# Optimization experiments

Measured on AMD Instinct MI355X. Metric: run time of the kernel, lower is better.

Reference implementation:

```python
import jax, jax.numpy as jnp
import numpy as np

FSIZE = 128   # fsize
ANUM = 16     # number of agents
CNUM = 2048   # number of cities
BATCH = 64


def setup_inputs() -> dict:
    key = jax.random.key(0)
    ks = jax.random.split(key, 6)
    f = FSIZE
    N = CNUM + 2 * ANUM
    s = 0.02
    return {
        "nfeature": jax.random.normal(ks[0], (BATCH, f, N), jnp.float32),
        # torch Linear weights are [out, in]
        "Wg": jax.random.normal(ks[1], (f, 4 * f), jnp.float32) * s,   # glb_embedding
        "bg": jnp.zeros((f,), jnp.float32),
        "Wc": jax.random.normal(ks[2], (3 * f, 2 * f), jnp.float32) * s,  # city_embedding
        "bc": jnp.zeros((3 * f,), jnp.float32),
        "Wa": jax.random.normal(ks[3], (f, 3 * f), jnp.float32) * s,   # agent_embedding
        "ba": jnp.zeros((f,), jnp.float32),
        "Wp": jax.random.normal(ks[4], (f, f), jnp.float32) * s,       # project_out
        "bp": jnp.zeros((f,), jnp.float32),
        "step": 1,
        "anum": ANUM,
    }


def reference(nfeature, Wg, bg, Wc, bc, Wa, ba, Wp, bp, step, anum):
    nf = jnp.transpose(nfeature, (0, 2, 1))  # [B, N, f]
    B, N, f = nf.shape
    cnum = N - 2 * anum
    city = nf[:, :cnum]                       # [B, cnum, f]
    a_start = nf[:, cnum:cnum + anum]         # [B, anum, f]
    a_end = nf[:, cnum + anum:]               # [B, anum, f]

    # global context via max pooling over segments -> glb_embedding
    glb = jnp.concatenate([nf.max(1), city.max(1), a_start.max(1), a_end.max(1)], axis=1)  # [B, 4f]
    deglb = (glb @ Wg.T + bg)[:, None, :]     # [B, 1, f]

    # mean-pooled global context -> same glb_embedding -> free agent token
    ave = jnp.concatenate([nf.mean(1), city.mean(1), a_start.mean(1), a_end.mean(1)], axis=1)
    free_agent = (ave @ Wg.T + bg)[:, None, :]  # [B, 1, f]

    # city keys/values/logit-keys: x, y, z
    city_feat = jnp.concatenate([jnp.broadcast_to(deglb, (B, cnum, f)), city], axis=2)  # [B, cnum, 2f]
    xyz = city_feat @ Wc.T + bc               # [B, cnum, 3f]
    x, y, z = jnp.split(xyz, 3, axis=2)       # each [B, cnum, f]

    # agent queries
    agent_feat = jnp.concatenate(
        [jnp.broadcast_to(deglb, (B, anum, f)), a_start, a_end], axis=2)  # [B, anum, 3f]
    af = agent_feat @ Wa.T + ba               # [B, anum, f]
    if step > 0:
        af = jnp.concatenate([af, free_agent], axis=1)  # [B, anum+1, f]

    scale = 1.0 / jnp.sqrt(jnp.float32(f))
    ucj = jnp.einsum('baf,bcf->bac', af, x) * scale           # [B, A, cnum]
    new_af = jnp.einsum('bac,bcf->baf', jax.nn.softmax(ucj, axis=2), y)
    new_af = new_af @ Wp.T + bp                                # project_out
    logits = jnp.tanh(jnp.einsum('baf,bcf->bac', new_af, z) * scale) * 10.0  # [B, A, cnum]
    probs = jax.nn.softmax(jnp.transpose(logits, (0, 2, 1)), axis=2)         # [B, cnum, A]
    return probs
```

## Files before the change

### kernel.cpp

```cpp
#include <hip/hip_runtime.h>
#include <math.h>

#define F 128
#define NTOT 2080
#define CN 2048
#define AN 16
#define NA 17

__device__ __forceinline__ float wmax(float v){
  #pragma unroll
  for(int m=32;m;m>>=1) v = fmaxf(v, __shfl_xor(v, m, 64));
  return v;
}
__device__ __forceinline__ float wsum(float v){
  #pragma unroll
  for(int m=32;m;m>>=1) v += __shfl_xor(v, m, 64);
  return v;
}

__global__ __launch_bounds__(256) void k0t_transpose(
      const float* __restrict__ Wg, const float* __restrict__ Wc,
      const float* __restrict__ Wp, const float* __restrict__ Wa,
      float* __restrict__ WgT, float* __restrict__ WcT,
      float* __restrict__ WpT, float* __restrict__ WaT){
  __shared__ float tile[32][33];
  const int z = blockIdx.z;
  const float* src; float* dst; int R, C;
  if(z==0){ src=Wg; dst=WgT; R=128; C=512; }
  else if(z==1){ src=Wc; dst=WcT; R=384; C=256; }
  else if(z==2){ src=Wp; dst=WpT; R=128; C=128; }
  else { src=Wa; dst=WaT; R=128; C=384; }
  const int c0 = blockIdx.x*32, r0 = blockIdx.y*32;
  if(c0>=C || r0>=R) return;
  const int tx = threadIdx.x&31, ty = threadIdx.x>>5;
  #pragma unroll
  for(int rr=0;rr<4;rr++)
    tile[ty+rr*8][tx] = src[(size_t)(r0+ty+rr*8)*C + c0 + tx];
  __syncthreads();
  #pragma unroll
  for(int rr=0;rr<4;rr++)
    dst[(size_t)(c0+ty+rr*8)*R + r0 + tx] = tile[tx][ty+rr*8];
}

__global__ __launch_bounds__(128) void k0a_wpy(const float* __restrict__ Wp, const float* __restrict__ Wc,
                                               float* __restrict__ Wpy){
  const int k = blockIdx.x, i = threadIdx.x;
  float acc = 0.f;
  const float* wp = Wp + (size_t)k*F;
  for(int j=0;j<F;j++) acc += wp[j]*Wc[(size_t)(128+j)*256 + 128 + i];
  Wpy[k*F+i] = acc;
}

__global__ __launch_bounds__(128) void k0b_m1(const float* __restrict__ Wc, const float* __restrict__ Wpy,
                                              float* __restrict__ M1){
  const int jc = blockIdx.x, i = threadIdx.x;
  float acc = 0.f;
  for(int k=0;k<F;k++) acc += Wc[(size_t)(256+k)*256 + 128 + jc]*Wpy[k*F+i];
  M1[jc*F+i] = acc;
}

__global__ __launch_bounds__(256) void k1_reduce(const float* __restrict__ nf,
                                                 float* __restrict__ glb, float* __restrict__ ave){
  const int j = blockIdx.x, b = blockIdx.y, tid = threadIdx.x;
  const float4* row = (const float4*)(nf + (size_t)(b*F + j)*NTOT);
  float cmax=-INFINITY, csum=0.f, smax=-INFINITY, ssum=0.f, emax=-INFINITY, esum=0.f;
  for(int n4 = tid; n4 < 520; n4 += 256){
    float4 v = row[n4];
    float mx = fmaxf(fmaxf(v.x,v.y), fmaxf(v.z,v.w));
    float sm = (v.x+v.y)+(v.z+v.w);
    if(n4 < 512){ cmax=fmaxf(cmax,mx); csum+=sm; }
    else if(n4 < 516){ smax=fmaxf(smax,mx); ssum+=sm; }
    else { emax=fmaxf(emax,mx); esum+=sm; }
  }
  __shared__ float red[4][6];
  cmax=wmax(cmax); csum=wsum(csum); smax=wmax(smax); ssum=wsum(ssum); emax=wmax(emax); esum=wsum(esum);
  const int lane = tid&63, wid = tid>>6;
  if(lane==0){ red[wid][0]=cmax; red[wid][1]=csum; red[wid][2]=smax; red[wid][3]=ssum; red[wid][4]=emax; red[wid][5]=esum; }
  __syncthreads();
  if(tid==0){
    float cM=red[0][0], cS=red[0][1], sM=red[0][2], sS=red[0][3], eM=red[0][4], eS=red[0][5];
    for(int w=1;w<4;w++){ cM=fmaxf(cM,red[w][0]); cS+=red[w][1]; sM=fmaxf(sM,red[w][2]); sS+=red[w][3]; eM=fmaxf(eM,red[w][4]); eS+=red[w][5]; }
    const int gb = b*4*F;
    glb[gb + j]       = fmaxf(cM, fmaxf(sM,eM));
    glb[gb + F + j]   = cM;
    glb[gb + 2*F + j] = sM;
    glb[gb + 3*F + j] = eM;
    float tS = cS+sS+eS;
    ave[gb + j]       = tS / 2080.f;
    ave[gb + F + j]   = cS / 2048.f;
    ave[gb + 2*F + j] = sS / 16.f;
    ave[gb + 3*F + j] = eS / 16.f;
  }
}

__global__ __launch_bounds__(256) void k2a_prep(
    const float* __restrict__ WgT, const float* __restrict__ bg,
    const float* __restrict__ WcT, const float* __restrict__ Wc, const float* __restrict__ bc,
    const float* __restrict__ WpT, const float* __restrict__ bp,
    const float* __restrict__ Wpy,
    const float* __restrict__ glb, const float* __restrict__ ave,
    float* __restrict__ deglb_g, float* __restrict__ fa_g, float* __restrict__ cx,
    float* __restrict__ czc, float* __restrict__ vz, float* __restrict__ szc){
  const int b = blockIdx.x, tid = threadIdx.x;
  __shared__ float glb_s[512], ave_s[512];
  __shared__ float deglb_s[F], cvec_s[3*F], cpy_s[F];
  for(int i=tid;i<512;i+=256){ glb_s[i]=glb[b*512+i]; ave_s[i]=ave[b*512+i]; }
  __syncthreads();
  {
    const int j = tid&127;
    const float* src = (tid<128)? glb_s : ave_s;
    float a0=0.f,a1=0.f,a2=0.f,a3=0.f;
    for(int k=0;k<512;k+=4){
      a0 += WgT[(size_t)(k+0)*128+j]*src[k+0];
      a1 += WgT[(size_t)(k+1)*128+j]*src[k+1];
      a2 += WgT[(size_t)(k+2)*128+j]*src[k+2];
      a3 += WgT[(size_t)(k+3)*128+j]*src[k+3];
    }
    float d = (a0+a1)+(a2+a3) + bg[j];
    if(tid<128){ deglb_s[j]=d; deglb_g[b*F+j]=d; }
    else fa_g[b*F+j]=d;
  }
  __syncthreads();
  for(int i=tid;i<3*F;i+=256){
    float a0=0.f,a1=0.f,a2=0.f,a3=0.f;
    for(int k=0;k<F;k+=4){
      a0 += WcT[(size_t)(k+0)*384+i]*deglb_s[k+0];
      a1 += WcT[(size_t)(k+1)*384+i]*deglb_s[k+1];
      a2 += WcT[(size_t)(k+2)*384+i]*deglb_s[k+2];
      a3 += WcT[(size_t)(k+3)*384+i]*deglb_s[k+3];
    }
    float v = (a0+a1)+(a2+a3) + bc[i];
    cvec_s[i]=v;
    if(i<F) cx[b*F+i]=v;
  }
  __syncthreads();
  if(tid<128){
    const int j = tid;
    float a0=0.f,a1=0.f,a2=0.f,a3=0.f;
    for(int k=0;k<F;k+=4){
      a0 += WpT[(size_t)(k+0)*128+j]*cvec_s[128+k+0];
      a1 += WpT[(size_t)(k+1)*128+j]*cvec_s[128+k+1];
      a2 += WpT[(size_t)(k+2)*128+j]*cvec_s[128+k+2];
      a3 += WpT[(size_t)(k+3)*128+j]*cvec_s[128+k+3];
    }
    cpy_s[j] = (a0+a1)+(a2+a3) + bp[j];
  } else {
    const int j = tid-128;
    float a0=0.f,a1=0.f,a2=0.f,a3=0.f;
    for(int k=0;k<F;k+=4){
      a0 += Wpy[(size_t)(k+0)*128+j]*cvec_s[256+k+0];
      a1 += Wpy[(size_t)(k+1)*128+j]*cvec_s[256+k+1];
      a2 += Wpy[(size_t)(k+2)*128+j]*cvec_s[256+k+2];
      a3 += Wpy[(size_t)(k+3)*128+j]*cvec_s[256+k+3];
    }
    vz[b*F+j] = (a0+a1)+(a2+a3);
  }
  __syncthreads();
  if(tid<128){
    const int j = tid;
    float a0=0.f,a1=0.f,a2=0.f,a3=0.f;
    for(int k=0;k<F;k+=4){
      a0 += Wc[(size_t)(256+k+0)*256 + 128 + j]*cpy_s[k+0];
      a1 += Wc[(size_t)(256+k+1)*256 + 128 + j]*cpy_s[k+1];
      a2 += Wc[(size_t)(256+k+2)*256 + 128 + j]*cpy_s[k+2];
      a3 += Wc[(size_t)(256+k+3)*256 + 128 + j]*cpy_s[k+3];
    }
    czc[b*F+j] = (a0+a1)+(a2+a3);
  } else if(tid<192){
    const int lane = tid-128;
    float p = cpy_s[lane]*cvec_s[256+lane] + cpy_s[64+lane]*cvec_s[256+64+lane];
    p = wsum(p);
    if(lane==0) szc[b]=p;
  }
}

__global__ __launch_bounds__(256) void k2c_agents(
    const float* __restrict__ nf, const float* __restrict__ WaT, const float* __restrict__ ba,
    const float* __restrict__ Wc,
    const float* __restrict__ deglb_g, const float* __restrict__ fa_g, const float* __restrict__ cx,
    float* __restrict__ afx, float* __restrict__ sx){
  const int a = blockIdx.x, b = blockIdx.y, tid = threadIdx.x;
  __shared__ float src_s[384];
  __shared__ float af_s[F], cx_s[F];
  if(tid<128){ src_s[tid] = deglb_g[b*F+tid]; cx_s[tid]=cx[b*F+tid]; }
  else if(a<16){
    const int j = tid-128;
    src_s[128+j] = nf[(size_t)(b*F+j)*NTOT + CN + a];
    src_s[256+j] = nf[(size_t)(b*F+j)*NTOT + CN + AN + a];
  }
  __syncthreads();
  if(a<16){
    if(tid<128){
      const int j = tid;
      float a0=0.f,a1=0.f,a2=0.f,a3=0.f;
      for(int k=0;k<384;k+=4){
        a0 += WaT[(size_t)(k+0)*128+j]*src_s[k+0];
        a1 += WaT[(size_t)(k+1)*128+j]*src_s[k+1];
        a2 += WaT[(size_t)(k+2)*128+j]*src_s[k+2];
        a3 += WaT[(size_t)(k+3)*128+j]*src_s[k+3];
      }
      af_s[j] = (a0+a1)+(a2+a3) + ba[j];
    }
  } else if(tid<128){
    af_s[tid] = fa_g[b*F+tid];
  }
  __syncthreads();
  if(tid<128){
    const int j = tid;
    float a0=0.f,a1=0.f,a2=0.f,a3=0.f;
    for(int i=0;i<F;i+=4){
      a0 += af_s[i+0]*Wc[(size_t)(i+0)*256 + 128 + j];
      a1 += af_s[i+1]*Wc[(size_t)(i+1)*256 + 128 + j];
      a2 += af_s[i+2]*Wc[(size_t)(i+2)*256 + 128 + j];
      a3 += af_s[i+3]*Wc[(size_t)(i+3)*256 + 128 + j];
    }
    afx[((size_t)b*NA+a)*F + j] = (a0+a1)+(a2+a3);
  } else if(tid<192){
    const int lane = tid-128;
    float p = af_s[lane]*cx_s[lane] + af_s[64+lane]*cx_s[64+lane];
    p = wsum(p);
    if(lane==0) sx[b*NA+a]=p;
  }
}

__global__ __launch_bounds__(256) void k35_flash(const float* __restrict__ nf,
      const float* __restrict__ afx, const float* __restrict__ sx,
      float* __restrict__ pmax, float* __restrict__ psum, float* __restrict__ tpart){
  const int b = blockIdx.y, tid = threadIdx.x;
  const int chunk = blockIdx.x, c0 = chunk*256;
  __shared__ float afx_s[NA*F];
  __shared__ float sx_s[NA];
  __shared__ float at_s[NA*256];
  __shared__ float4 nf4_s[F*16];
  __shared__ float red_s[4][NA];
  __shared__ float m_s[NA];
  for(int o=tid;o<NA*F;o+=256) afx_s[o]=afx[(size_t)b*NA*F+o];
  if(tid<NA) sx_s[tid]=sx[b*NA+tid];
  __syncthreads();
  float acc[NA];
  #pragma unroll
  for(int a=0;a<NA;a++) acc[a]=0.f;
  {
    const float* base = nf + (size_t)b*F*NTOT + c0 + tid;
    #pragma unroll 4
    for(int i=0;i<F;i++){
      float v = base[(size_t)i*NTOT];
      #pragma unroll
      for(int a=0;a<NA;a++) acc[a] += afx_s[a*F+i]*v;
    }
  }
  const float scale = 0.088388347648318447f;
  #pragma unroll
  for(int a=0;a<NA;a++) acc[a] = (acc[a]+sx_s[a])*scale;
  const int lane = tid&63, wid = tid>>6;
  #pragma unroll
  for(int a=0;a<NA;a++){
    float m = wmax(acc[a]);
    if(lane==0) red_s[wid][a]=m;
  }
  __syncthreads();
  if(tid<NA){
    float m = fmaxf(fmaxf(red_s[0][tid],red_s[1][tid]), fmaxf(red_s[2][tid],red_s[3][tid]));
    m_s[tid]=m;
    pmax[(b*NA+tid)*8 + chunk]=m;
  }
  __syncthreads();
  #pragma unroll
  for(int a=0;a<NA;a++){
    float e = __expf(acc[a]-m_s[a]);
    at_s[a*256+tid]=e;
    float s = wsum(e);
    if(lane==0) red_s[wid][a]=s;
  }
  __syncthreads();
  if(tid<NA)
    psum[(b*NA+tid)*8 + chunk] = red_s[0][tid]+red_s[1][tid]+red_s[2][tid]+red_s[3][tid];
  const int i = tid&127, h = tid>>7, A0 = h*8;
  float ta[9];
  #pragma unroll
  for(int a=0;a<9;a++) ta[a]=0.f;
  for(int s4=0;s4<4;s4++){
    const int cs = c0 + s4*64;
    __syncthreads();
    for(int idx=tid; idx<F*16; idx+=256){
      const int ii=idx>>4, g=idx&15;
      nf4_s[ii*16 + (g^(ii&15))] = *(const float4*)(nf + (size_t)(b*F+ii)*NTOT + cs + g*4);
    }
    __syncthreads();
    #pragma unroll 2
    for(int g=0; g<16; g++){
      float4 v = nf4_s[i*16 + (g^(i&15))];
      #pragma unroll
      for(int a=0;a<9;a++){
        float4 w = *(const float4*)&at_s[(A0+a)*256 + s4*64 + g*4];
        ta[a] += w.x*v.x + w.y*v.y + w.z*v.z + w.w*v.w;
      }
    }
  }
  float* dst = tpart + (size_t)chunk*64*NA*F + (size_t)b*NA*F;
  #pragma unroll
  for(int a=0;a<9;a++){
    if(h==0 || a>0) dst[(A0+a)*F + i] = ta[a];
  }
}

__global__ __launch_bounds__(128) void k5c_final(const float* __restrict__ M1,
      const float* __restrict__ tpart, const float* __restrict__ pmax, const float* __restrict__ psum,
      const float* __restrict__ czc, const float* __restrict__ vz, const float* __restrict__ szc,
      float* __restrict__ afz, float* __restrict__ szv){
  const int a = blockIdx.x, b = blockIdx.y, tid = threadIdx.x;
  __shared__ float tn_s[F];
  const float* pm = pmax + (b*NA+a)*8;
  const float* ps = psum + (b*NA+a)*8;
  float M=-INFINITY;
  #pragma unroll
  for(int k=0;k<8;k++) M = fmaxf(M, pm[k]);
  float w[8]; float rs=0.f;
  #pragma unroll
  for(int k=0;k<8;k++){ w[k]=__expf(pm[k]-M); rs += ps[k]*w[k]; }
  float s = 0.f;
  #pragma unroll
  for(int k=0;k<8;k++) s += tpart[(size_t)k*64*NA*F + ((size_t)b*NA+a)*F + tid]*w[k];
  tn_s[tid] = s / rs;
  __syncthreads();
  float acc = 0.f;
  const float* m = M1 + (size_t)tid*F;
  for(int i=0;i<F;i++) acc += m[i]*tn_s[i];
  afz[((size_t)b*NA+a)*F + tid] = acc + czc[b*F+tid];
  float p = tn_s[tid]*vz[b*F+tid];
  p = wsum(p);
  __shared__ float red[2];
  if((tid&63)==0) red[tid>>6]=p;
  __syncthreads();
  if(tid==0) szv[b*NA+a] = red[0]+red[1] + szc[b];
}

__global__ __launch_bounds__(256) void k6_out(const float* __restrict__ nf, const float* __restrict__ afz,
      const float* __restrict__ szv, const int* __restrict__ step, float* __restrict__ out){
  const int b = blockIdx.y, tid = threadIdx.x;
  const int c = blockIdx.x*256 + tid;
  __shared__ float afz_s[NA*F]; __shared__ float sz_s[NA];
  for(int o=tid;o<NA*F;o+=256) afz_s[o]=afz[(size_t)b*NA*F+o];
  if(tid<NA) sz_s[tid]=szv[b*NA+tid];
  __syncthreads();
  const int A = (step[0] > 0) ? NA : AN;
  float acc[NA];
  #pragma unroll
  for(int a=0;a<NA;a++) acc[a]=0.f;
  const float* base = nf + (size_t)b*F*NTOT + c;
  #pragma unroll 4
  for(int i=0;i<F;i++){
    float v = base[(size_t)i*NTOT];
    #pragma unroll
    for(int a=0;a<NA;a++) acc[a] += afz_s[a*F+i]*v;
  }
  const float scale = 0.088388347648318447f;
  float l[NA];
  #pragma unroll
  for(int a=0;a<NA;a++) l[a] = tanhf((acc[a]+sz_s[a])*scale)*10.f;
  const bool f17 = (A==NA);
  float m = l[0];
  #pragma unroll
  for(int a=1;a<AN;a++) m = fmaxf(m,l[a]);
  if(f17) m = fmaxf(m,l[16]);
  float ssum=0.f;
  #pragma unroll
  for(int a=0;a<AN;a++){ float e=__expf(l[a]-m); l[a]=e; ssum+=e; }
  float e16=__expf(l[16]-m);
  if(f17){ ssum+=e16; }
  const float inv = 1.f/ssum;
  float* op = out + (size_t)(b*CN + c)*A;
  #pragma unroll
  for(int a=0;a<AN;a++) op[a]=l[a]*inv;
  if(f17) op[16]=e16*inv;
}

extern "C" void kernel_launch(void* const* d_in, const int* in_sizes, int n_in,
                              void* d_out, int out_size, void* d_ws, size_t ws_size,
                              hipStream_t stream){
  const float* nf = (const float*)d_in[0];
  const float* Wg = (const float*)d_in[1];
  const float* bg = (const float*)d_in[2];
  const float* Wc = (const float*)d_in[3];
  const float* bc = (const float*)d_in[4];
  const float* Wa = (const float*)d_in[5];
  const float* ba = (const float*)d_in[6];
  const float* Wp = (const float*)d_in[7];
  const float* bp = (const float*)d_in[8];
  const int*  step = (const int*)d_in[9];
  float* out = (float*)d_out;

  float* ws = (float*)d_ws;
  float* glb     = ws;
  float* ave     = glb + 64*512;
  float* afx     = ave + 64*512;
  float* sx      = afx + 64*NA*F;
  float* Wpy     = sx + 64*NA;
  float* M1      = Wpy + F*F;
  float* czc     = M1 + F*F;
  float* vz      = czc + 64*F;
  float* szc     = vz + 64*F;
  float* pmax    = szc + 64;
  float* psum    = pmax + 64*NA*8;
  float* deglb_g = psum + 64*NA*8;
  float* fa_g    = deglb_g + 64*F;
  float* cx      = fa_g + 64*F;
  float* WgT     = cx + 64*F;
  float* WcT     = WgT + 512*F;
  float* WpT     = WcT + 256*384;
  float* WaT     = WpT + F*F;
  float* tpart   = WaT + 384*F;
  float* afz     = tpart + 8*64*NA*F;
  float* szv     = afz + 64*NA*F;

  k0t_transpose<<<dim3(16,12,4),256,0,stream>>>(Wg,Wc,Wp,Wa, WgT,WcT,WpT,WaT);
  k0a_wpy<<<F,F,0,stream>>>(Wp, Wc, Wpy);
  k0b_m1<<<F,F,0,stream>>>(Wc, Wpy, M1);
  k1_reduce<<<dim3(128,64),256,0,stream>>>(nf, glb, ave);
  k2a_prep<<<64,256,0,stream>>>(WgT,bg, WcT,Wc,bc, WpT,bp, Wpy, glb,ave, deglb_g,fa_g,cx, czc,vz,szc);
  k2c_agents<<<dim3(NA,64),256,0,stream>>>(nf, WaT,ba,Wc, deglb_g,fa_g,cx, afx,sx);
  k35_flash<<<dim3(8,64),256,0,stream>>>(nf, afx, sx, pmax, psum, tpart);
  k5c_final<<<dim3(NA,64),128,0,stream>>>(M1, tpart, pmax, psum, czc, vz, szc, afz, szv);
  k6_out<<<dim3(8,64),256,0,stream>>>(nf, afz, szv, step, out);
}
```

Baseline: 158.0 us.

## Halve city chunk size and split feature dimension across half-blocks in flash and output kernels

Shrinks the city chunk per block from 256 to 128 so the flash and output kernels launch twice as many blocks. Within each block, the two 128-thread halves each compute a partial dot product over half of the 128 features using float4 weight loads, then combine the halves through shared memory. The reduce kernel now maps one wavefront per feature row and drops its shared-memory block reduction. The aim is more occupancy and parallelism on the memory-bound passes, at the cost of more partial results (tpart, pmax, psum) for the final merge kernel and half the threads idling during the softmax and output phases.

```diff
diff --git a/kernel.cpp b/kernel.cpp
--- a/kernel.cpp
+++ b/kernel.cpp
@@ -6,6 +6,8 @@
 #define CN 2048
 #define AN 16
 #define NA 17
+#define CHK 128
+#define NCHK 16
 
 __device__ __forceinline__ float wmax(float v){
   #pragma unroll
@@ -61,10 +63,12 @@
 
 __global__ __launch_bounds__(256) void k1_reduce(const float* __restrict__ nf,
                                                  float* __restrict__ glb, float* __restrict__ ave){
-  const int j = blockIdx.x, b = blockIdx.y, tid = threadIdx.x;
+  const int jg = blockIdx.x, b = blockIdx.y;
+  const int w = threadIdx.x>>6, lane = threadIdx.x&63;
+  const int j = jg*4 + w;
   const float4* row = (const float4*)(nf + (size_t)(b*F + j)*NTOT);
   float cmax=-INFINITY, csum=0.f, smax=-INFINITY, ssum=0.f, emax=-INFINITY, esum=0.f;
-  for(int n4 = tid; n4 < 520; n4 += 256){
+  for(int n4 = lane; n4 < 520; n4 += 64){
     float4 v = row[n4];
     float mx = fmaxf(fmaxf(v.x,v.y), fmaxf(v.z,v.w));
     float sm = (v.x+v.y)+(v.z+v.w);
@@ -72,24 +76,18 @@
     else if(n4 < 516){ smax=fmaxf(smax,mx); ssum+=sm; }
     else { emax=fmaxf(emax,mx); esum+=sm; }
   }
-  __shared__ float red[4][6];
   cmax=wmax(cmax); csum=wsum(csum); smax=wmax(smax); ssum=wsum(ssum); emax=wmax(emax); esum=wsum(esum);
-  const int lane = tid&63, wid = tid>>6;
-  if(lane==0){ red[wid][0]=cmax; red[wid][1]=csum; red[wid][2]=smax; red[wid][3]=ssum; red[wid][4]=emax; red[wid][5]=esum; }
-  __syncthreads();
-  if(tid==0){
-    float cM=red[0][0], cS=red[0][1], sM=red[0][2], sS=red[0][3], eM=red[0][4], eS=red[0][5];
-    for(int w=1;w<4;w++){ cM=fmaxf(cM,red[w][0]); cS+=red[w][1]; sM=fmaxf(sM,red[w][2]); sS+=red[w][3]; eM=fmaxf(eM,red[w][4]); eS+=red[w][5]; }
+  if(lane==0){
     const int gb = b*4*F;
-    glb[gb + j]       = fmaxf(cM, fmaxf(sM,eM));
-    glb[gb + F + j]   = cM;
-    glb[gb + 2*F + j] = sM;
-    glb[gb + 3*F + j] = eM;
-    float tS = cS+sS+eS;
+    glb[gb + j]       = fmaxf(cmax, fmaxf(smax,emax));
+    glb[gb + F + j]   = cmax;
+    glb[gb + 2*F + j] = smax;
+    glb[gb + 3*F + j] = emax;
+    float tS = csum+ssum+esum;
     ave[gb + j]       = tS / 2080.f;
-    ave[gb + F + j]   = cS / 2048.f;
-    ave[gb + 2*F + j] = sS / 16.f;
-    ave[gb + 3*F + j] = eS / 16.f;
+    ave[gb + F + j]   = csum / 2048.f;
+    ave[gb + 2*F + j] = ssum / 16.f;
+    ave[gb + 3*F + j] = esum / 16.f;
   }
 }
 
@@ -227,72 +225,88 @@
       const float* __restrict__ afx, const float* __restrict__ sx,
       float* __restrict__ pmax, float* __restrict__ psum, float* __restrict__ tpart){
   const int b = blockIdx.y, tid = threadIdx.x;
-  const int chunk = blockIdx.x, c0 = chunk*256;
+  const int chunk = blockIdx.x, c0 = chunk*CHK;
   __shared__ float afx_s[NA*F];
   __shared__ float sx_s[NA];
-  __shared__ float at_s[NA*256];
-  __shared__ float4 nf4_s[F*16];
-  __shared__ float red_s[4][NA];
+  __shared__ float at_s[NA*CHK];
+  __shared__ float4 nf4_s[F*8];
+  __shared__ float red_s[2][NA];
   __shared__ float m_s[NA];
   for(int o=tid;o<NA*F;o+=256) afx_s[o]=afx[(size_t)b*NA*F+o];
   if(tid<NA) sx_s[tid]=sx[b*NA+tid];
   __syncthreads();
+  const int h = tid>>7, cl = tid&127, i0 = h*64;
   float acc[NA];
   #pragma unroll
   for(int a=0;a<NA;a++) acc[a]=0.f;
   {
-    const float* base = nf + (size_t)b*F*NTOT + c0 + tid;
-    #pragma unroll 4
-    for(int i=0;i<F;i++){
-      float v = base[(size_t)i*NTOT];
+    const float* base = nf + (size_t)b*F*NTOT + (size_t)i0*NTOT + c0 + cl;
+    for(int q=0;q<16;q++){
+      float v0 = base[(size_t)(q*4+0)*NTOT];
+      float v1 = base[(size_t)(q*4+1)*NTOT];
+      float v2 = base[(size_t)(q*4+2)*NTOT];
+      float v3 = base[(size_t)(q*4+3)*NTOT];
       #pragma unroll
-      for(int a=0;a<NA;a++) acc[a] += afx_s[a*F+i]*v;
-    }
-  }
+      for(int a=0;a<NA;a++){
+        float4 w = *(const float4*)&afx_s[a*F + i0 + q*4];
+        acc[a] += w.x*v0 + w.y*v1 + w.z*v2 + w.w*v3;
+      }
+    }
+  }
+  if(h==0){
+    #pragma unroll
+    for(int a=0;a<NA;a++) at_s[a*CHK+cl] = acc[a];
+  }
+  __syncthreads();
+  const int lane = tid&63;
   const float scale = 0.088388347648318447f;
-  #pragma unroll
-  for(int a=0;a<NA;a++) acc[a] = (acc[a]+sx_s[a])*scale;
-  const int lane = tid&63, wid = tid>>6;
-  #pragma unroll
-  for(int a=0;a<NA;a++){
-    float m = wmax(acc[a]);
-    if(lane==0) red_s[wid][a]=m;
+  if(h==1){
+    const int wq = (tid>>6)&1;
+    #pragma unroll
+    for(int a=0;a<NA;a++){
+      acc[a] = (acc[a] + at_s[a*CHK+cl] + sx_s[a])*scale;
+      float m = wmax(acc[a]);
+      if(lane==0) red_s[wq][a]=m;
+    }
   }
   __syncthreads();
   if(tid<NA){
-    float m = fmaxf(fmaxf(red_s[0][tid],red_s[1][tid]), fmaxf(red_s[2][tid],red_s[3][tid]));
+    float m = fmaxf(red_s[0][tid], red_s[1][tid]);
     m_s[tid]=m;
-    pmax[(b*NA+tid)*8 + chunk]=m;
-  }
-  __syncthreads();
-  #pragma unroll
-  for(int a=0;a<NA;a++){
-    float e = __expf(acc[a]-m_s[a]);
-    at_s[a*256+tid]=e;
-    float s = wsum(e);
-    if(lane==0) red_s[wid][a]=s;
+    pmax[(b*NA+tid)*NCHK + chunk]=m;
+  }
+  __syncthreads();
+  if(h==1){
+    const int wq = (tid>>6)&1;
+    #pragma unroll
+    for(int a=0;a<NA;a++){
+      float e = __expf(acc[a]-m_s[a]);
+      at_s[a*CHK+cl]=e;
+      float s = wsum(e);
+      if(lane==0) red_s[wq][a]=s;
+    }
   }
   __syncthreads();
   if(tid<NA)
-    psum[(b*NA+tid)*8 + chunk] = red_s[0][tid]+red_s[1][tid]+red_s[2][tid]+red_s[3][tid];
-  const int i = tid&127, h = tid>>7, A0 = h*8;
+    psum[(b*NA+tid)*NCHK + chunk] = red_s[0][tid]+red_s[1][tid];
+  const int i = tid&127, A0 = h*8;
   float ta[9];
   #pragma unroll
   for(int a=0;a<9;a++) ta[a]=0.f;
   for(int s4=0;s4<4;s4++){
-    const int cs = c0 + s4*64;
+    const int csl = s4*32, cs = c0 + csl;
     __syncthreads();
-    for(int idx=tid; idx<F*16; idx+=256){
-      const int ii=idx>>4, g=idx&15;
-      nf4_s[ii*16 + (g^(ii&15))] = *(const float4*)(nf + (size_t)(b*F+ii)*NTOT + cs + g*4);
+    for(int idx=tid; idx<F*8; idx+=256){
+      const int ii=idx>>3, g=idx&7;
+      nf4_s[ii*8 + (g^(ii&7))] = *(const float4*)(nf + (size_t)(b*F+ii)*NTOT + cs + g*4);
     }
     __syncthreads();
     #pragma unroll 2
-    for(int g=0; g<16; g++){
-      float4 v = nf4_s[i*16 + (g^(i&15))];
+    for(int g=0; g<8; g++){
+      float4 v = nf4_s[i*8 + (g^(i&7))];
       #pragma unroll
       for(int a=0;a<9;a++){
-        float4 w = *(const float4*)&at_s[(A0+a)*256 + s4*64 + g*4];
+        float4 w = *(const float4*)&at_s[(A0+a)*CHK + csl + g*4];
         ta[a] += w.x*v.x + w.y*v.y + w.z*v.z + w.w*v.w;
       }
     }
@@ -310,17 +324,17 @@
       float* __restrict__ afz, float* __restrict__ szv){
   const int a = blockIdx.x, b = blockIdx.y, tid = threadIdx.x;
   __shared__ float tn_s[F];
-  const float* pm = pmax + (b*NA+a)*8;
-  const float* ps = psum + (b*NA+a)*8;
+  const float* pm = pmax + (b*NA+a)*NCHK;
+  const float* ps = psum + (b*NA+a)*NCHK;
   float M=-INFINITY;
   #pragma unroll
-  for(int k=0;k<8;k++) M = fmaxf(M, pm[k]);
-  float w[8]; float rs=0.f;
-  #pragma unroll
-  for(int k=0;k<8;k++){ w[k]=__expf(pm[k]-M); rs += ps[k]*w[k]; }
+  for(int k=0;k<NCHK;k++) M = fmaxf(M, pm[k]);
+  float w[NCHK]; float rs=0.f;
+  #pragma unroll
+  for(int k=0;k<NCHK;k++){ w[k]=__expf(pm[k]-M); rs += ps[k]*w[k]; }
   float s = 0.f;
   #pragma unroll
-  for(int k=0;k<8;k++) s += tpart[(size_t)k*64*NA*F + ((size_t)b*NA+a)*F + tid]*w[k];
+  for(int k=0;k<NCHK;k++) s += tpart[(size_t)k*64*NA*F + ((size_t)b*NA+a)*F + tid]*w[k];
   tn_s[tid] = s / rs;
   __syncthreads();
   float acc = 0.f;
@@ -338,41 +352,58 @@
 __global__ __launch_bounds__(256) void k6_out(const float* __restrict__ nf, const float* __restrict__ afz,
       const float* __restrict__ szv, const int* __restrict__ step, float* __restrict__ out){
   const int b = blockIdx.y, tid = threadIdx.x;
-  const int c = blockIdx.x*256 + tid;
+  const int chunk = blockIdx.x, c0 = chunk*CHK;
   __shared__ float afz_s[NA*F]; __shared__ float sz_s[NA];
+  __shared__ float sc_s[NA*CHK];
   for(int o=tid;o<NA*F;o+=256) afz_s[o]=afz[(size_t)b*NA*F+o];
   if(tid<NA) sz_s[tid]=szv[b*NA+tid];
   __syncthreads();
-  const int A = (step[0] > 0) ? NA : AN;
+  const int h = tid>>7, cl = tid&127, i0 = h*64;
   float acc[NA];
   #pragma unroll
   for(int a=0;a<NA;a++) acc[a]=0.f;
-  const float* base = nf + (size_t)b*F*NTOT + c;
-  #pragma unroll 4
-  for(int i=0;i<F;i++){
-    float v = base[(size_t)i*NTOT];
-    #pragma unroll
-    for(int a=0;a<NA;a++) acc[a] += afz_s[a*F+i]*v;
-  }
-  const float scale = 0.088388347648318447f;
-  float l[NA];
-  #pragma unroll
-  for(int a=0;a<NA;a++) l[a] = tanhf((acc[a]+sz_s[a])*scale)*10.f;
-  const bool f17 = (A==NA);
-  float m = l[0];
-  #pragma unroll
-  for(int a=1;a<AN;a++) m = fmaxf(m,l[a]);
-  if(f17) m = fmaxf(m,l[16]);
-  float ssum=0.f;
-  #pragma unroll
-  for(int a=0;a<AN;a++){ float e=__expf(l[a]-m); l[a]=e; ssum+=e; }
-  float e16=__expf(l[16]-m);
-  if(f17){ ssum+=e16; }
-  const float inv = 1.f/ssum;
-  float* op = out + (size_t)(b*CN + c)*A;
-  #pragma unroll
-  for(int a=0;a<AN;a++) op[a]=l[a]*inv;
-  if(f17) op[16]=e16*inv;
+  {
+    const float* base = nf + (size_t)b*F*NTOT + (size_t)i0*NTOT + c0 + cl;
+    for(int q=0;q<16;q++){
+      float v0 = base[(size_t)(q*4+0)*NTOT];
+      float v1 = base[(size_t)(q*4+1)*NTOT];
+      float v2 = base[(size_t)(q*4+2)*NTOT];
+      float v3 = base[(size_t)(q*4+3)*NTOT];
+      #pragma unroll
+      for(int a=0;a<NA;a++){
+        float4 w = *(const float4*)&afz_s[a*F + i0 + q*4];
+        acc[a] += w.x*v0 + w.y*v1 + w.z*v2 + w.w*v3;
+      }
+    }
+  }
+  if(h==0){
+    #pragma unroll
+    for(int a=0;a<NA;a++) sc_s[a*CHK+cl] = acc[a];
+  }
+  __syncthreads();
+  if(h==1){
+    const int A = (step[0] > 0) ? NA : AN;
+    const float scale = 0.088388347648318447f;
+    float l[NA];
+    #pragma unroll
+    for(int a=0;a<NA;a++)
+      l[a] = tanhf((acc[a] + sc_s[a*CHK+cl] + sz_s[a])*scale)*10.f;
+    const bool f17 = (A==NA);
+    float m = l[0];
+    #pragma unroll
+    for(int a=1;a<AN;a++) m = fmaxf(m,l[a]);
+    if(f17) m = fmaxf(m,l[16]);
+    float ssum=0.f;
+    #pragma unroll
+    for(int a=0;a<AN;a++){ float e=__expf(l[a]-m); l[a]=e; ssum+=e; }
+    float e16=__expf(l[16]-m);
+    if(f17){ ssum+=e16; }
+    const float inv = 1.f/ssum;
+    float* op = out + (size_t)(b*CN + c0 + cl)*A;
+    #pragma unroll
+    for(int a=0;a<AN;a++) op[a]=l[a]*inv;
+    if(f17) op[16]=e16*inv;
+  }
 }
 
 extern "C" void kernel_launch(void* const* d_in, const int* in_sizes, int n_in,
@@ -401,8 +432,8 @@
   float* vz      = czc + 64*F;
   float* szc     = vz + 64*F;
   float* pmax    = szc + 64;
-  float* psum    = pmax + 64*NA*8;
-  float* deglb_g = psum + 64*NA*8;
+  float* psum    = pmax + 64*NA*NCHK;
+  float* deglb_g = psum + 64*NA*NCHK;
   float* fa_g    = deglb_g + 64*F;
   float* cx      = fa_g + 64*F;
   float* WgT     = cx + 64*F;
@@ -410,16 +441,16 @@
   float* WpT     = WcT + 256*384;
   float* WaT     = WpT + F*F;
   float* tpart   = WaT + 384*F;
-  float* afz     = tpart + 8*64*NA*F;
+  float* afz     = tpart + (size_t)NCHK*64*NA*F;
   float* szv     = afz + 64*NA*F;
 
   k0t_transpose<<<dim3(16,12,4),256,0,stream>>>(Wg,Wc,Wp,Wa, WgT,WcT,WpT,WaT);
   k0a_wpy<<<F,F,0,stream>>>(Wp, Wc, Wpy);
   k0b_m1<<<F,F,0,stream>>>(Wc, Wpy, M1);
-  k1_reduce<<<dim3(128,64),256,0,stream>>>(nf, glb, ave);
+  k1_reduce<<<dim3(32,64),256,0,stream>>>(nf, glb, ave);
   k2a_prep<<<64,256,0,stream>>>(WgT,bg, WcT,Wc,bc, WpT,bp, Wpy, glb,ave, deglb_g,fa_g,cx, czc,vz,szc);
   k2c_agents<<<dim3(NA,64),256,0,stream>>>(nf, WaT,ba,Wc, deglb_g,fa_g,cx, afx,sx);
-  k35_flash<<<dim3(8,64),256,0,stream>>>(nf, afx, sx, pmax, psum, tpart);
+  k35_flash<<<dim3(NCHK,64),256,0,stream>>>(nf, afx, sx, pmax, psum, tpart);
   k5c_final<<<dim3(NA,64),128,0,stream>>>(M1, tpart, pmax, psum, czc, vz, szc, afz, szv);
-  k6_out<<<dim3(8,64),256,0,stream>>>(nf, afz, szv, step, out);
-}
+  k6_out<<<dim3(NCHK,64),256,0,stream>>>(nf, afz, szv, step, out);
+}
```

New measurement: 153.0 us (median of 2 runs). -3.1%, faster.
